# Optimization experiments

Hardware: AMD Instinct MI355X
Metric: run time of the kernel (lower is better)

Reference implementation:

```python
import jax, jax.numpy as jnp
import numpy as np

D = 768          # model dim (ViT-Base)
H = 12           # num heads
DH = 64          # head dim
DFF = 4 * D      # mlp hidden
SMAX = 1024      # max sequence length in the packed batch
LENS = np.array([1024, 896, 768, 640, 512, 448, 256, 64], dtype=np.int32)
TOTAL = int(LENS.sum())  # 4608
LN_EPS = 1e-6
NEG = -1e30


def _ln(x, w, b):
    mu = jnp.mean(x, axis=-1, keepdims=True)
    var = jnp.mean(jnp.square(x - mu), axis=-1, keepdims=True)
    return (x - mu) * jax.lax.rsqrt(var + LN_EPS) * w + b


def setup_inputs() -> dict:
    key = jax.random.key(0)
    ks = jax.random.split(key, 16)
    s = 0.02
    cu = jnp.asarray(np.concatenate([[0], np.cumsum(LENS)]).astype(np.int32))
    return {
        "x": jax.random.normal(ks[0], (TOTAL, D), jnp.float32),
        "norm1_w": jnp.ones((D,), jnp.float32),
        "norm1_b": jnp.zeros((D,), jnp.float32),
        "qkv_w": jax.random.normal(ks[1], (3 * D, D), jnp.float32) * s,
        "qkv_b": jnp.zeros((3 * D,), jnp.float32),
        "proj_w": jax.random.normal(ks[2], (D, D), jnp.float32) * s,
        "proj_b": jnp.zeros((D,), jnp.float32),
        "ls1_gamma": jax.random.normal(ks[3], (D,), jnp.float32) * 0.1,
        "norm2_w": jnp.ones((D,), jnp.float32),
        "norm2_b": jnp.zeros((D,), jnp.float32),
        "fc1_w": jax.random.normal(ks[4], (DFF, D), jnp.float32) * s,
        "fc1_b": jnp.zeros((DFF,), jnp.float32),
        "fc2_w": jax.random.normal(ks[5], (D, DFF), jnp.float32) * s,
        "fc2_b": jnp.zeros((D,), jnp.float32),
        "ls2_gamma": jax.random.normal(ks[6], (D,), jnp.float32) * 0.1,
        "cu_seqlens": cu,
    }


def reference(x, norm1_w, norm1_b, qkv_w, qkv_b, proj_w, proj_b, ls1_gamma,
              norm2_w, norm2_b, fc1_w, fc1_b, fc2_w, fc2_b, ls2_gamma,
              cu_seqlens):
    total = x.shape[0]
    B = cu_seqlens.shape[0] - 1
    tok = jnp.arange(total)
    seg = jnp.searchsorted(cu_seqlens[1:], tok, side="right")  # [Total]
    pos = tok - cu_seqlens[seg]                                 # [Total]
    lens = cu_seqlens[1:] - cu_seqlens[:-1]                     # [B]

    # --- attention branch ---
    xn = _ln(x, norm1_w, norm1_b)
    qkv = (xn @ qkv_w.T + qkv_b).reshape(total, 3, H, DH)
    q, k, v = qkv[:, 0], qkv[:, 1], qkv[:, 2]                   # [Total,H,DH]

    # pad packed ragged tokens to [B, SMAX, H, DH]
    def pad(t):
        return jnp.zeros((B, SMAX, H, DH), t.dtype).at[seg, pos].set(t)
    qp, kp, vp = pad(q), pad(k), pad(v)

    valid = jnp.arange(SMAX)[None, :] < lens[:, None]           # [B,SMAX]
    scores = jnp.einsum("bqhd,bkhd->bhqk", qp, kp) * (DH ** -0.5)
    scores = jnp.where(valid[:, None, None, :], scores, NEG)
    attn = jax.nn.softmax(scores, axis=-1)
    out = jnp.einsum("bhqk,bkhd->bqhd", attn, vp)
    out = out[seg, pos].reshape(total, D)                       # back to packed

    attn_out = out @ proj_w.T + proj_b
    x = x + ls1_gamma * attn_out

    # --- mlp branch ---
    xn2 = _ln(x, norm2_w, norm2_b)
    h = jax.nn.gelu(xn2 @ fc1_w.T + fc1_b, approximate=False)
    h = h @ fc2_w.T + fc2_b
    return x + ls2_gamma * h
```

## Files before the change

### kernel.cpp

```cpp
#include <hip/hip_runtime.h>
#include <hip/hip_bf16.h>
#include <stdint.h>

#define D 768
#define HEADS 12
#define DHEAD 64
#define DFF 3072
#define TOTAL 4608
#define NSEG 8

typedef __bf16 bf16;
typedef __bf16 bf16x8 __attribute__((ext_vector_type(8)));
typedef __bf16 bf16x4 __attribute__((ext_vector_type(4)));
typedef float f32x4 __attribute__((ext_vector_type(4)));

#define NSLOT 221
#define PSTRIDE 4352

__device__ __forceinline__ void gld_lds16(const void* g, void* l) {
  __builtin_amdgcn_global_load_lds(
      (const __attribute__((address_space(1))) void*)g,
      (__attribute__((address_space(3))) void*)(uintptr_t)l, 16, 0, 0);
}

__device__ __forceinline__ void lds_barrier() {
  asm volatile("s_waitcnt lgkmcnt(0)\n\ts_barrier" ::: "memory");
}

__global__ __launch_bounds__(256) void cvt_all_kernel(
    const float* __restrict__ a, const float* __restrict__ b,
    const float* __restrict__ c, const float* __restrict__ d,
    bf16* __restrict__ out, int nA, int nAB, int nABC, int nTot) {
  int i = blockIdx.x * blockDim.x + threadIdx.x;
  if (i >= nTot) return;
  const float* src;
  int j;
  if (i < nA) { src = a; j = i; }
  else if (i < nAB) { src = b; j = i - nA; }
  else if (i < nABC) { src = c; j = i - nAB; }
  else { src = d; j = i - nABC; }
  float4 v = ((const float4*)src)[j];
  bf16x4 o;
  o[0] = (bf16)v.x; o[1] = (bf16)v.y; o[2] = (bf16)v.z; o[3] = (bf16)v.w;
  ((bf16x4*)out)[i] = o;
}

__global__ __launch_bounds__(256) void ln_kernel(
    const float* __restrict__ x, const float* __restrict__ w,
    const float* __restrict__ b, bf16* __restrict__ out) {
  __shared__ float red[8];
  int row = blockIdx.x;
  const float* xr = x + (size_t)row * D;
  int t = threadIdx.x;
  float v[3];
  float s = 0.f, s2 = 0.f;
#pragma unroll
  for (int j = 0; j < 3; j++) {
    v[j] = xr[t + 256 * j];
    s += v[j]; s2 += v[j] * v[j];
  }
#pragma unroll
  for (int m = 1; m <= 32; m <<= 1) {
    s += __shfl_xor(s, m);
    s2 += __shfl_xor(s2, m);
  }
  int wave = t >> 6, lane = t & 63;
  if (lane == 0) { red[wave] = s; red[4 + wave] = s2; }
  __syncthreads();
  s = red[0] + red[1] + red[2] + red[3];
  s2 = red[4] + red[5] + red[6] + red[7];
  float mu = s * (1.f / 768.f);
  float var = s2 * (1.f / 768.f) - mu * mu;
  float rstd = rsqrtf(var + 1e-6f);
#pragma unroll
  for (int j = 0; j < 3; j++) {
    int c = t + 256 * j;
    out[(size_t)row * D + c] = (bf16)((v[j] - mu) * rstd * w[c] + b[c]);
  }
}

__device__ __forceinline__ float fast_gelu(float v) {
  float u = v * (0.7978845608f + 0.0356774081f * v * v);
  float e = exp2f(2.8853900818f * u);
  float th = 1.f - 2.f * __builtin_amdgcn_rcpf(1.f + e);
  return 0.5f * v * (1.f + th);
}

template <int MODE, int TN, int BK, int GX, int GY>
__global__ __launch_bounds__(256) void gemm_kernel(
    const bf16* __restrict__ A, const bf16* __restrict__ W,
    const float* __restrict__ bias, const float* __restrict__ res,
    const float* __restrict__ gamma, bf16* __restrict__ outb,
    float* __restrict__ outf, int N, int K) {
  constexpr int NJ = TN / 32;
  constexpr int KH = BK / 32;
  constexpr int CG = BK / 8;
  constexpr int SH = (BK == 32) ? 1 : 0;
  constexpr int LPR = BK / 8;
  constexpr int RS = 64 / LPR;
  constexpr int RB = TN / 4;
  constexpr int NSTG = 32 / RS + RB / RS;
  __shared__ __align__(16) bf16 As[2][128 * BK];
  __shared__ __align__(16) bf16 Bs[2][TN * BK];

  const int g = blockIdx.x;
  const int xc = g & 7, q = g >> 3;
  const int bx = q % GX, by = xc + 8 * (q / GX);
  if (by >= GY) return;
  const int m0 = by * 128, n0 = bx * TN;

  const int t = threadIdx.x, wave = t >> 6, lane = t & 63;
  const int quad = lane >> 4, l16 = lane & 15;
  const int wm = (wave & 1) * 64, wn = (wave >> 1) * (TN / 2);

  const int ar = lane / LPR, ac = lane % LPR;
  const int acg = ac ^ (((wave * 32 + ar) >> SH) & (CG - 1));
  const int bcg = ac ^ (((wave * RB + ar) >> SH) & (CG - 1));
  const bf16* gA = A + (size_t)(m0 + wave * 32 + ar) * K + acg * 8;
  const bf16* gB = W + (size_t)(n0 + wave * RB + ar) * K + bcg * 8;

  auto stage = [&](int buf) {
#pragma unroll
    for (int n = 0; n < 32 / RS; n++)
      gld_lds16(gA + (size_t)n * RS * K, &As[buf][(wave * 32 + n * RS) * BK]);
#pragma unroll
    for (int n = 0; n < RB / RS; n++)
      gld_lds16(gB + (size_t)n * RS * K, &Bs[buf][(wave * RB + n * RS) * BK]);
    gA += BK; gB += BK;
  };

  stage(0);

  f32x4 acc[4][NJ] = {};
  int cur = 0;
  for (int k0 = 0; k0 < K; k0 += BK) {
    if (k0 + BK < K) {
      asm volatile("s_waitcnt lgkmcnt(0)\n\ts_barrier" ::: "memory");
      stage(cur ^ 1);
      if constexpr (NSTG == 8)
        asm volatile("s_waitcnt vmcnt(8)\n\ts_barrier" ::: "memory");
      else
        asm volatile("s_waitcnt vmcnt(6)\n\ts_barrier" ::: "memory");
    } else {
      asm volatile("s_waitcnt vmcnt(0)\n\ts_barrier" ::: "memory");
    }
    const bf16* as = As[cur];
    const bf16* bs = Bs[cur];
    bf16x8 af[KH][4], bg[KH][NJ];
#pragma unroll
    for (int kh = 0; kh < KH; kh++) {
#pragma unroll
      for (int i = 0; i < 4; i++) {
        int R = wm + i * 16 + l16;
        af[kh][i] = *(const bf16x8*)&as[R * BK + 8 * ((kh * 4 + quad) ^ ((R >> SH) & (CG - 1)))];
      }
#pragma unroll
      for (int j = 0; j < NJ; j++) {
        int R = wn + j * 16 + l16;
        bg[kh][j] = *(const bf16x8*)&bs[R * BK + 8 * ((kh * 4 + quad) ^ ((R >> SH) & (CG - 1)))];
      }
    }
#pragma unroll
    for (int kh = 0; kh < KH; kh++)
#pragma unroll
      for (int i = 0; i < 4; i++)
#pragma unroll
        for (int j = 0; j < NJ; j++)
          acc[i][j] = __builtin_amdgcn_mfma_f32_16x16x32_bf16(af[kh][i], bg[kh][j], acc[i][j], 0, 0, 0);
    cur ^= 1;
  }

#pragma unroll
  for (int i = 0; i < 4; i++)
#pragma unroll
    for (int j = 0; j < NJ; j++)
#pragma unroll
      for (int r = 0; r < 4; r++) {
        int row = m0 + wm + i * 16 + quad * 4 + r;
        int col = n0 + wn + j * 16 + l16;
        float v = acc[i][j][r] + bias[col];
        if (MODE == 0) {
          outb[(size_t)row * N + col] = (bf16)v;
        } else if (MODE == 1) {
          outf[(size_t)row * N + col] = res[(size_t)row * N + col] + gamma[col] * v;
        } else {
          outb[(size_t)row * N + col] = (bf16)fast_gelu(v);
        }
      }
}

__global__ __launch_bounds__(256) void attn_part_kernel(
    const bf16* __restrict__ qkv, float* __restrict__ part) {
  __shared__ __align__(16) bf16 Ks[2][64][72];
  __shared__ __align__(16) bf16 VTs[2][64][64];

  const int NTt[8] = {16, 14, 12, 10, 8, 7, 4, 1};
  const int NCt[8] = {4, 4, 3, 3, 2, 2, 1, 1};
  const int BSt[8] = {0, 64, 120, 156, 186, 202, 216, 220};
  const int CU0[8] = {0, 1024, 1920, 2688, 3328, 3840, 4288, 4544};

  const int x = blockIdx.x, h = blockIdx.y;
  int s = 0;
#pragma unroll
  for (int i = 1; i < 8; i++) if (x >= BSt[i]) s = i;
  const int r0 = x - BSt[s];
  const int qt = r0 / NCt[s], c = r0 % NCt[s];
  const int s0 = CU0[s];
  const int tok0 = s0 + qt * 64;
  const int tb = c * 4;
  const int te = min(tb + 4, NTt[s]);
  const int n = te - tb;

  const int t = threadIdx.x, wave = t >> 6, lane = t & 63;
  const int quad = lane >> 4, l16 = lane & 15;

  const size_t qrow = (size_t)(tok0 + wave * 16 + l16) * (3 * D) + h * 64;
  const bf16x8 bq0 = *(const bf16x8*)&qkv[qrow + quad * 8];
  const bf16x8 bq1 = *(const bf16x8*)&qkv[qrow + 32 + quad * 8];

  const int srow = t >> 2, sc0 = (t & 3) * 16;
  const size_t kbase = (size_t)(s0 + srow) * (3 * D) + h * 64 + sc0 + D;
  const int vr0 = (t & 15) * 4, vd0 = (t >> 4) * 4;
  const size_t vbase = (size_t)(s0 + vr0) * (3 * D) + h * 64 + vd0 + 2 * D;
  const int kB0 = ((vr0 >> 5) << 5) | (((vr0 >> 2) & 3) << 3) | (((vr0 >> 4) & 1) << 2);

  f32x4 Oacc[4] = {};
  float li = 0.f;
  const float SC = 0.125f * 1.44269504089f;

  bf16x8 kA0, kA1, kB0r, kB1r;
  bf16x4 vA[4], vB[4];

  auto loadT = [&](int tile, bf16x8& k0, bf16x8& k1, bf16x4* vp) {
    const size_t ko = kbase + (size_t)tile * 64 * (3 * D);
    const size_t vo = vbase + (size_t)tile * 64 * (3 * D);
    k0 = *(const bf16x8*)&qkv[ko];
    k1 = *(const bf16x8*)&qkv[ko + 8];
#pragma unroll
    for (int i = 0; i < 4; i++)
      vp[i] = *(const bf16x4*)&qkv[vo + (size_t)i * (3 * D)];
  };
  auto writeT = [&](int buf, const bf16x8& k0, const bf16x8& k1, const bf16x4* vp) {
    *(bf16x8*)&Ks[buf][srow][sc0] = k0;
    *(bf16x8*)&Ks[buf][srow][sc0 + 8] = k1;
#pragma unroll
    for (int j = 0; j < 4; j++) {
      int d = vd0 + j;
      bf16x4 w;
      w[0] = vp[0][j]; w[1] = vp[1][j]; w[2] = vp[2][j]; w[3] = vp[3][j];
      *(bf16x4*)&VTs[buf][d][kB0 ^ ((d & 7) * 8)] = w;
    }
  };
  auto computeT = [&](int buf) {
    f32x4 sac[4];
#pragma unroll
    for (int nt = 0; nt < 4; nt++) {
      bf16x8 ak0 = *(const bf16x8*)&Ks[buf][nt * 16 + l16][quad * 8];
      bf16x8 ak1 = *(const bf16x8*)&Ks[buf][nt * 16 + l16][32 + quad * 8];
      f32x4 z = {};
      z = __builtin_amdgcn_mfma_f32_16x16x32_bf16(ak0, bq0, z, 0, 0, 0);
      sac[nt] = __builtin_amdgcn_mfma_f32_16x16x32_bf16(ak1, bq1, z, 0, 0, 0);
    }
    bf16x8 pv0, pv1;
    float ls = 0.f;
#pragma unroll
    for (int r = 0; r < 4; r++) {
      float e0 = exp2f(sac[0][r] * SC);
      float e1 = exp2f(sac[1][r] * SC);
      float e2 = exp2f(sac[2][r] * SC);
      float e3 = exp2f(sac[3][r] * SC);
      ls += (e0 + e1) + (e2 + e3);
      pv0[r] = (bf16)e0; pv0[4 + r] = (bf16)e1;
      pv1[r] = (bf16)e2; pv1[4 + r] = (bf16)e3;
    }
    li += ls;
    const int vsw = (l16 & 7) * 8;
#pragma unroll
    for (int dt = 0; dt < 4; dt++) {
      bf16x8 av0 = *(const bf16x8*)&VTs[buf][dt * 16 + l16][(quad * 8) ^ vsw];
      bf16x8 av1 = *(const bf16x8*)&VTs[buf][dt * 16 + l16][(32 + quad * 8) ^ vsw];
      Oacc[dt] = __builtin_amdgcn_mfma_f32_16x16x32_bf16(av0, pv0, Oacc[dt], 0, 0, 0);
      Oacc[dt] = __builtin_amdgcn_mfma_f32_16x16x32_bf16(av1, pv1, Oacc[dt], 0, 0, 0);
    }
  };

  loadT(tb, kA0, kA1, vA);
  if (n > 1) loadT(tb + 1, kB0r, kB1r, vB);
  writeT(0, kA0, kA1, vA);

  for (int tt = 0; tt < n; tt += 2) {
    lds_barrier();
    if (tt + 1 < n) writeT(1, kB0r, kB1r, vB);
    if (tt + 2 < n) loadT(tb + tt + 2, kA0, kA1, vA);
    computeT(0);
    if (tt + 1 >= n) break;
    lds_barrier();
    if (tt + 2 < n) writeT(0, kA0, kA1, vA);
    if (tt + 3 < n) loadT(tb + tt + 3, kB0r, kB1r, vB);
    computeT(1);
  }

  li += __shfl_xor(li, 16);
  li += __shfl_xor(li, 32);
  float* pb = part + ((size_t)x * HEADS + h) * PSTRIDE;
#pragma unroll
  for (int dt = 0; dt < 4; dt++)
    *(f32x4*)&pb[dt * 1024 + t * 4] = Oacc[dt];
  pb[4096 + t] = li;
}

__global__ __launch_bounds__(256) void attn_comb_kernel(
    const float* __restrict__ part, bf16* __restrict__ attn) {
  __shared__ __align__(16) bf16 Osh[64][72];
  const int NCt[8] = {4, 4, 3, 3, 2, 2, 1, 1};
  const int BSt[8] = {0, 64, 120, 156, 186, 202, 216, 220};
  const int STt[8] = {0, 16, 30, 42, 52, 60, 67, 71};

  const int qt = blockIdx.x, h = blockIdx.y;
  int s = 0;
#pragma unroll
  for (int i = 1; i < 8; i++) if (qt >= STt[i]) s = i;
  const int qtl = qt - STt[s];
  const int nc = NCt[s];
  const float* pb = part + ((size_t)(BSt[s] + qtl * nc) * HEADS + h) * PSTRIDE;

  const int t = threadIdx.x, wave = t >> 6, lane = t & 63;
  const int quad = lane >> 4, l16 = lane & 15;

  f32x4 O[4] = {};
  float li = 0.f;
  for (int c = 0; c < nc; c++) {
    const float* p = pb + (size_t)c * HEADS * PSTRIDE;
#pragma unroll
    for (int dt = 0; dt < 4; dt++) {
      f32x4 v = *(const f32x4*)&p[dt * 1024 + t * 4];
      O[dt][0] += v[0]; O[dt][1] += v[1]; O[dt][2] += v[2]; O[dt][3] += v[3];
    }
    li += p[4096 + t];
  }
  const float inv = 1.f / li;

  const int orow = wave * 16 + l16;
  const int osw = (l16 & 7) * 8;
#pragma unroll
  for (int dt = 0; dt < 4; dt++) {
    int dg = dt * 16 + quad * 4;
    bf16x4 w;
#pragma unroll
    for (int r = 0; r < 4; r++) w[r] = (bf16)(O[dt][r] * inv);
    *(bf16x4*)&Osh[orow][dg ^ osw] = w;
  }
  bf16x8 o0 = *(const bf16x8*)&Osh[orow][(quad * 16) ^ osw];
  bf16x8 o1 = *(const bf16x8*)&Osh[orow][(quad * 16 + 8) ^ osw];
  const size_t ob = (size_t)(qt * 64 + orow) * D + h * 64 + quad * 16;
  *(bf16x8*)&attn[ob] = o0;
  *(bf16x8*)&attn[ob + 8] = o1;
}

extern "C" void kernel_launch(void* const* d_in, const int* in_sizes, int n_in,
                              void* d_out, int out_size, void* d_ws,
                              size_t ws_size, hipStream_t stream) {
  const float* x       = (const float*)d_in[0];
  const float* norm1_w = (const float*)d_in[1];
  const float* norm1_b = (const float*)d_in[2];
  const float* qkv_w   = (const float*)d_in[3];
  const float* qkv_b   = (const float*)d_in[4];
  const float* proj_w  = (const float*)d_in[5];
  const float* proj_b  = (const float*)d_in[6];
  const float* ls1     = (const float*)d_in[7];
  const float* norm2_w = (const float*)d_in[8];
  const float* norm2_b = (const float*)d_in[9];
  const float* fc1_w   = (const float*)d_in[10];
  const float* fc1_b   = (const float*)d_in[11];
  const float* fc2_w   = (const float*)d_in[12];
  const float* fc2_b   = (const float*)d_in[13];
  const float* ls2     = (const float*)d_in[14];
  float* out = (float*)d_out;

  char* ws = (char*)d_ws;
  size_t off = 0;
  auto alloc = [&](size_t bytes) {
    void* p = ws + off;
    off += (bytes + 255) & ~(size_t)255;
    return p;
  };
  bf16* w_qkv  = (bf16*)alloc((size_t)3 * D * D * 2);
  bf16* w_proj = (bf16*)alloc((size_t)D * D * 2);
  bf16* w_fc1  = (bf16*)alloc((size_t)DFF * D * 2);
  bf16* w_fc2  = (bf16*)alloc((size_t)D * DFF * 2);
  bf16* xn     = (bf16*)alloc((size_t)TOTAL * D * 2);
  bf16* qkv    = (bf16*)alloc((size_t)TOTAL * 3 * D * 2);
  bf16* attnb  = (bf16*)alloc((size_t)TOTAL * D * 2);
  float* x1    = (float*)alloc((size_t)TOTAL * D * 4);
  float* part  = (float*)alloc((size_t)NSLOT * HEADS * PSTRIDE * 4);
  bf16* hbuf   = qkv;

  {
    int nA   = 3 * D * D / 4;
    int nAB  = nA + D * D / 4;
    int nABC = nAB + DFF * D / 4;
    int nTot = nABC + D * DFF / 4;
    cvt_all_kernel<<<(nTot + 255) / 256, 256, 0, stream>>>(
        qkv_w, proj_w, fc1_w, fc2_w, w_qkv, nA, nAB, nABC, nTot);
  }

  ln_kernel<<<TOTAL, 256, 0, stream>>>(x, norm1_w, norm1_b, xn);

  constexpr int GY = TOTAL / 128;
  constexpr int GYP = ((GY + 7) / 8) * 8;

  gemm_kernel<0, 128, 64, 18, GY><<<18 * GYP, 256, 0, stream>>>(
      xn, w_qkv, qkv_b, nullptr, nullptr, qkv, nullptr, 3 * D, D);

  dim3 gp(NSLOT, HEADS);
  attn_part_kernel<<<gp, 256, 0, stream>>>(qkv, part);
  dim3 gc(TOTAL / 64, HEADS);
  attn_comb_kernel<<<gc, 256, 0, stream>>>(part, attnb);

  gemm_kernel<1, 64, 64, 12, GY><<<12 * GYP, 256, 0, stream>>>(
      attnb, w_proj, proj_b, x, ls1, nullptr, x1, D, D);

  ln_kernel<<<TOTAL, 256, 0, stream>>>(x1, norm2_w, norm2_b, xn);

  gemm_kernel<2, 128, 64, 24, GY><<<24 * GYP, 256, 0, stream>>>(
      xn, w_fc1, fc1_b, nullptr, nullptr, hbuf, nullptr, DFF, D);

  gemm_kernel<1, 64, 64, 12, GY><<<12 * GYP, 256, 0, stream>>>(
      hbuf, w_fc2, fc2_b, x1, ls2, nullptr, out, D, DFF);
}
```

Baseline: 272.3 us.

## Preload all attention K/V tiles upfront via LDS DMA; store partials in bf16

The attention partial kernel drops the double-buffered load/compute pipeline. It now issues every K tile (up to 4) as direct global-to-LDS loads with an XOR swizzle and loads every V tile into registers, transposes V into LDS, then runs one barrier before an unsynchronised compute loop. The partial outputs passed to the combine kernel are stored in bf16 instead of fp32, roughly halving that write and read traffic. The cost is larger LDS use (4 tiles for K and V), which may lower occupancy, and some loss of precision in the partial sums.

Result: slower. 842.0 us (+209.2%).

```diff
diff --git a/kernel.cpp b/kernel.cpp
--- a/kernel.cpp
+++ b/kernel.cpp
@@ -15,16 +15,12 @@
 typedef float f32x4 __attribute__((ext_vector_type(4)));
 
 #define NSLOT 221
-#define PSTRIDE 4352
+#define PSTB 4608
 
 __device__ __forceinline__ void gld_lds16(const void* g, void* l) {
   __builtin_amdgcn_global_load_lds(
       (const __attribute__((address_space(1))) void*)g,
       (__attribute__((address_space(3))) void*)(uintptr_t)l, 16, 0, 0);
-}
-
-__device__ __forceinline__ void lds_barrier() {
-  asm volatile("s_waitcnt lgkmcnt(0)\n\ts_barrier" ::: "memory");
 }
 
 __global__ __launch_bounds__(256) void cvt_all_kernel(
@@ -190,9 +186,9 @@
 }
 
 __global__ __launch_bounds__(256) void attn_part_kernel(
-    const bf16* __restrict__ qkv, float* __restrict__ part) {
-  __shared__ __align__(16) bf16 Ks[2][64][72];
-  __shared__ __align__(16) bf16 VTs[2][64][64];
+    const bf16* __restrict__ qkv, bf16* __restrict__ part) {
+  __shared__ __align__(16) bf16 Ks[4][64][64];
+  __shared__ __align__(16) bf16 VTs[4][64][64];
 
   const int NTt[8] = {16, 14, 12, 10, 8, 7, 4, 1};
   const int NCt[8] = {4, 4, 3, 3, 2, 2, 1, 1};
@@ -208,8 +204,7 @@
   const int s0 = CU0[s];
   const int tok0 = s0 + qt * 64;
   const int tb = c * 4;
-  const int te = min(tb + 4, NTt[s]);
-  const int n = te - tb;
+  const int n = min(4, NTt[s] - tb);
 
   const int t = threadIdx.x, wave = t >> 6, lane = t & 63;
   const int quad = lane >> 4, l16 = lane & 15;
@@ -218,45 +213,47 @@
   const bf16x8 bq0 = *(const bf16x8*)&qkv[qrow + quad * 8];
   const bf16x8 bq1 = *(const bf16x8*)&qkv[qrow + 32 + quad * 8];
 
-  const int srow = t >> 2, sc0 = (t & 3) * 16;
-  const size_t kbase = (size_t)(s0 + srow) * (3 * D) + h * 64 + sc0 + D;
+  const int ar = lane >> 3, ac = lane & 7;
   const int vr0 = (t & 15) * 4, vd0 = (t >> 4) * 4;
-  const size_t vbase = (size_t)(s0 + vr0) * (3 * D) + h * 64 + vd0 + 2 * D;
   const int kB0 = ((vr0 >> 5) << 5) | (((vr0 >> 2) & 3) << 3) | (((vr0 >> 4) & 1) << 2);
+
+  bf16x4 vreg[4][4];
+  for (int tt = 0; tt < n; tt++) {
+    const int kb = (tb + tt) * 64;
+#pragma unroll
+    for (int nn = 0; nn < 2; nn++) {
+      const int row = wave * 16 + nn * 8 + ar;
+      gld_lds16(&qkv[(size_t)(s0 + kb + row) * (3 * D) + h * 64 + D + (ac ^ ar) * 8],
+                &Ks[tt][wave * 16 + nn * 8][0]);
+    }
+    const size_t vb = (size_t)(s0 + kb + vr0) * (3 * D) + h * 64 + 2 * D + vd0;
+#pragma unroll
+    for (int i = 0; i < 4; i++)
+      vreg[tt][i] = *(const bf16x4*)&qkv[vb + (size_t)i * (3 * D)];
+  }
+  for (int tt = 0; tt < n; tt++) {
+#pragma unroll
+    for (int j = 0; j < 4; j++) {
+      int d = vd0 + j;
+      bf16x4 w;
+      w[0] = vreg[tt][0][j]; w[1] = vreg[tt][1][j];
+      w[2] = vreg[tt][2][j]; w[3] = vreg[tt][3][j];
+      *(bf16x4*)&VTs[tt][d][kB0 ^ ((d & 7) * 8)] = w;
+    }
+  }
+  __syncthreads();
 
   f32x4 Oacc[4] = {};
   float li = 0.f;
   const float SC = 0.125f * 1.44269504089f;
 
-  bf16x8 kA0, kA1, kB0r, kB1r;
-  bf16x4 vA[4], vB[4];
-
-  auto loadT = [&](int tile, bf16x8& k0, bf16x8& k1, bf16x4* vp) {
-    const size_t ko = kbase + (size_t)tile * 64 * (3 * D);
-    const size_t vo = vbase + (size_t)tile * 64 * (3 * D);
-    k0 = *(const bf16x8*)&qkv[ko];
-    k1 = *(const bf16x8*)&qkv[ko + 8];
-#pragma unroll
-    for (int i = 0; i < 4; i++)
-      vp[i] = *(const bf16x4*)&qkv[vo + (size_t)i * (3 * D)];
-  };
-  auto writeT = [&](int buf, const bf16x8& k0, const bf16x8& k1, const bf16x4* vp) {
-    *(bf16x8*)&Ks[buf][srow][sc0] = k0;
-    *(bf16x8*)&Ks[buf][srow][sc0 + 8] = k1;
-#pragma unroll
-    for (int j = 0; j < 4; j++) {
-      int d = vd0 + j;
-      bf16x4 w;
-      w[0] = vp[0][j]; w[1] = vp[1][j]; w[2] = vp[2][j]; w[3] = vp[3][j];
-      *(bf16x4*)&VTs[buf][d][kB0 ^ ((d & 7) * 8)] = w;
-    }
-  };
-  auto computeT = [&](int buf) {
+  for (int tt = 0; tt < n; tt++) {
     f32x4 sac[4];
 #pragma unroll
     for (int nt = 0; nt < 4; nt++) {
-      bf16x8 ak0 = *(const bf16x8*)&Ks[buf][nt * 16 + l16][quad * 8];
-      bf16x8 ak1 = *(const bf16x8*)&Ks[buf][nt * 16 + l16][32 + quad * 8];
+      const int R = nt * 16 + l16, sw = l16 & 7;
+      bf16x8 ak0 = *(const bf16x8*)&Ks[tt][R][8 * (quad ^ sw)];
+      bf16x8 ak1 = *(const bf16x8*)&Ks[tt][R][8 * ((4 + quad) ^ sw)];
       f32x4 z = {};
       z = __builtin_amdgcn_mfma_f32_16x16x32_bf16(ak0, bq0, z, 0, 0, 0);
       sac[nt] = __builtin_amdgcn_mfma_f32_16x16x32_bf16(ak1, bq1, z, 0, 0, 0);
@@ -277,40 +274,28 @@
     const int vsw = (l16 & 7) * 8;
 #pragma unroll
     for (int dt = 0; dt < 4; dt++) {
-      bf16x8 av0 = *(const bf16x8*)&VTs[buf][dt * 16 + l16][(quad * 8) ^ vsw];
-      bf16x8 av1 = *(const bf16x8*)&VTs[buf][dt * 16 + l16][(32 + quad * 8) ^ vsw];
+      bf16x8 av0 = *(const bf16x8*)&VTs[tt][dt * 16 + l16][(quad * 8) ^ vsw];
+      bf16x8 av1 = *(const bf16x8*)&VTs[tt][dt * 16 + l16][(32 + quad * 8) ^ vsw];
       Oacc[dt] = __builtin_amdgcn_mfma_f32_16x16x32_bf16(av0, pv0, Oacc[dt], 0, 0, 0);
       Oacc[dt] = __builtin_amdgcn_mfma_f32_16x16x32_bf16(av1, pv1, Oacc[dt], 0, 0, 0);
     }
-  };
-
-  loadT(tb, kA0, kA1, vA);
-  if (n > 1) loadT(tb + 1, kB0r, kB1r, vB);
-  writeT(0, kA0, kA1, vA);
-
-  for (int tt = 0; tt < n; tt += 2) {
-    lds_barrier();
-    if (tt + 1 < n) writeT(1, kB0r, kB1r, vB);
-    if (tt + 2 < n) loadT(tb + tt + 2, kA0, kA1, vA);
-    computeT(0);
-    if (tt + 1 >= n) break;
-    lds_barrier();
-    if (tt + 2 < n) writeT(0, kA0, kA1, vA);
-    if (tt + 3 < n) loadT(tb + tt + 3, kB0r, kB1r, vB);
-    computeT(1);
   }
 
   li += __shfl_xor(li, 16);
   li += __shfl_xor(li, 32);
-  float* pb = part + ((size_t)x * HEADS + h) * PSTRIDE;
-#pragma unroll
-  for (int dt = 0; dt < 4; dt++)
-    *(f32x4*)&pb[dt * 1024 + t * 4] = Oacc[dt];
-  pb[4096 + t] = li;
+  bf16* pb = part + ((size_t)x * HEADS + h) * PSTB;
+#pragma unroll
+  for (int dt = 0; dt < 4; dt++) {
+    bf16x4 w;
+#pragma unroll
+    for (int r = 0; r < 4; r++) w[r] = (bf16)Oacc[dt][r];
+    *(bf16x4*)&pb[dt * 1024 + t * 4] = w;
+  }
+  *(float*)&pb[4096 + 2 * t] = li;
 }
 
 __global__ __launch_bounds__(256) void attn_comb_kernel(
-    const float* __restrict__ part, bf16* __restrict__ attn) {
+    const bf16* __restrict__ part, bf16* __restrict__ attn) {
   __shared__ __align__(16) bf16 Osh[64][72];
   const int NCt[8] = {4, 4, 3, 3, 2, 2, 1, 1};
   const int BSt[8] = {0, 64, 120, 156, 186, 202, 216, 220};
@@ -322,7 +307,7 @@
   for (int i = 1; i < 8; i++) if (qt >= STt[i]) s = i;
   const int qtl = qt - STt[s];
   const int nc = NCt[s];
-  const float* pb = part + ((size_t)(BSt[s] + qtl * nc) * HEADS + h) * PSTRIDE;
+  const bf16* pb = part + ((size_t)(BSt[s] + qtl * nc) * HEADS + h) * PSTB;
 
   const int t = threadIdx.x, wave = t >> 6, lane = t & 63;
   const int quad = lane >> 4, l16 = lane & 15;
@@ -330,13 +315,14 @@
   f32x4 O[4] = {};
   float li = 0.f;
   for (int c = 0; c < nc; c++) {
-    const float* p = pb + (size_t)c * HEADS * PSTRIDE;
+    const bf16* p = pb + (size_t)c * HEADS * PSTB;
 #pragma unroll
     for (int dt = 0; dt < 4; dt++) {
-      f32x4 v = *(const f32x4*)&p[dt * 1024 + t * 4];
-      O[dt][0] += v[0]; O[dt][1] += v[1]; O[dt][2] += v[2]; O[dt][3] += v[3];
-    }
-    li += p[4096 + t];
+      bf16x4 v = *(const bf16x4*)&p[dt * 1024 + t * 4];
+      O[dt][0] += (float)v[0]; O[dt][1] += (float)v[1];
+      O[dt][2] += (float)v[2]; O[dt][3] += (float)v[3];
+    }
+    li += *(const float*)&p[4096 + 2 * t];
   }
   const float inv = 1.f / li;
 
@@ -392,7 +378,7 @@
   bf16* qkv    = (bf16*)alloc((size_t)TOTAL * 3 * D * 2);
   bf16* attnb  = (bf16*)alloc((size_t)TOTAL * D * 2);
   float* x1    = (float*)alloc((size_t)TOTAL * D * 4);
-  float* part  = (float*)alloc((size_t)NSLOT * HEADS * PSTRIDE * 4);
+  bf16* part   = (bf16*)alloc((size_t)NSLOT * HEADS * PSTB * 2);
   bf16* hbuf   = qkv;
 
   {
```
